# Kernel tuning notes

Measured on AMD Instinct MI355X. Metric: run time of the kernel, lower is better.

Reference implementation:

```python
import jax, jax.numpy as jnp
import numpy as np

KLD_BINS = 10
RATIO_KLD = 0.5
# categorical one-hot blocks in the 99-dim Adult encoding
BLOCKS = [(1, 8), (8, 24), (24, 31), (31, 45), (45, 51), (51, 53), (53, 55), (58, 99)]
CONT_COLS = np.array([0, 55, 56, 57])


def _cross_entropy(logits, onehot):
    # F.cross_entropy with targets = argmax of the one-hot block (mean over batch)
    logp = jax.nn.log_softmax(logits, axis=-1)
    return -jnp.mean(jnp.sum(onehot * logp, axis=-1))


def _kl_divergence(p, q):
    # np-style KL: sum p*log(p/q) over valid (nonzero) bins
    valid = (p > 0) & (q > 0)
    ratio = jnp.where(valid, p / jnp.where(valid, q, 1.0), 1.0)
    return jnp.sum(jnp.where(valid, p * jnp.log(ratio), 0.0))


def setup_inputs() -> dict:
    B = 262144
    key = jax.random.key(0)
    ks = jax.random.split(key, 16)
    data_decoded = jax.random.normal(ks[0], (B, 99), dtype=jnp.float32)
    # data_true: continuous columns + one-hot categorical blocks
    data_true = jnp.zeros((B, 99), dtype=jnp.float32)
    data_true = data_true.at[:, CONT_COLS].set(jax.random.normal(ks[1], (B, 4), dtype=jnp.float32))
    for j, (s, e) in enumerate(BLOCKS):
        lab = jax.random.randint(ks[2 + j], (B,), 0, e - s)
        data_true = data_true.at[:, s:e].set(jax.nn.one_hot(lab, e - s, dtype=jnp.float32))
    data_encoded = jax.random.normal(ks[11], (B, 12), dtype=jnp.float32)
    sex = jax.random.bernoulli(ks[12], 0.5, (B,)).astype(jnp.float32)
    data_encoded = data_encoded.at[:, 11].set(sex)  # column 11 of combined is the 0/1 sex neuron
    label_true = jax.random.normal(ks[13], (B, 2), dtype=jnp.float32)
    return {
        'data_encoded': data_encoded,
        'data_decoded': data_decoded,
        'data_true': data_true,
        'label_true': label_true,
        'batch_size': B,
    }


def reference(data_encoded, data_decoded, data_true, label_true, batch_size):
    # --- reconstruction MSE on continuous columns ---
    cc = jnp.asarray(CONT_COLS)
    mse_loss = jnp.sum(jnp.mean((data_decoded[:, cc] - data_true[:, cc]) ** 2, axis=0))
    # --- cross-entropy on each categorical block ---
    ce_loss = jnp.float32(0.0)
    for s, e in BLOCKS:
        ce_loss = ce_loss + _cross_entropy(data_decoded[:, s:e], data_true[:, s:e])
    # --- per-feature histogram KLD between male/female groups (no grad, as in torch via .numpy()) ---
    comb = jnp.concatenate([data_encoded, label_true], axis=1)  # [B, 14]
    feats = comb[:, :KLD_BINS]  # first 10 encoded features, [B, 10]
    mn = jnp.min(feats, axis=0)  # per-column min over full batch (torch .item())
    mx = jnp.max(feats, axis=0)
    width = jnp.maximum(mx - mn, 1e-12)
    # torch.histc bin index: floor((x-min)/(max-min)*bins), x==max -> last bin
    idx = jnp.clip(jnp.floor((feats - mn) / width * KLD_BINS).astype(jnp.int32), 0, KLD_BINS - 1)
    onehot = jax.nn.one_hot(idx, KLD_BINS, dtype=jnp.float32)  # [B, 10, bins]
    sexcol = comb[:, 11]
    m_mask = (sexcol == 0).astype(jnp.float32)
    f_mask = (sexcol == 1).astype(jnp.float32)
    m_count = jnp.maximum(jnp.sum(m_mask), 1.0)
    f_count = jnp.maximum(jnp.sum(f_mask), 1.0)
    m_hist = jnp.einsum('b,bik->ik', m_mask, onehot) / m_count  # [10, bins]
    f_hist = jnp.einsum('b,bik->ik', f_mask, onehot) / f_count
    kld = jax.lax.stop_gradient(_kl_divergence(m_hist, f_hist))
    alpha = RATIO_KLD
    multi_loss = (1.0 - alpha) * (mse_loss + ce_loss) + alpha * kld
    return (multi_loss, mse_loss, ce_loss, alpha * kld)
```

## Files before the change

### kernel.cpp

```cpp
#include <hip/hip_runtime.h>
#include <math.h>

#define B_ROWS 262144

#define WS_A 0
#define WS_B 2816
#define WS_C 28416
#define MAIN_BLOCKS 2048
#define N_TILES 4096

__device__ __forceinline__ unsigned int map_f(float x) {
  unsigned int b = __float_as_uint(x);
  return (b & 0x80000000u) ? ~b : (b | 0x80000000u);
}
__device__ __forceinline__ float unmap_f(unsigned int u) {
  unsigned int b = (u & 0x80000000u) ? (u ^ 0x80000000u) : ~u;
  return __uint_as_float(b);
}

__global__ __launch_bounds__(256) void k_minmax(const float* __restrict__ enc,
                                                unsigned int* __restrict__ ws) {
  int tid = threadIdx.x, bid = blockIdx.x;
  const float4* e4 = (const float4*)enc;
  float mn[10], mx[10];
  #pragma unroll
  for (int j = 0; j < 10; j++) { mn[j] = 1e30f; mx[j] = -1e30f; }
  unsigned int cm = 0, cf = 0;
  #pragma unroll
  for (int i = 0; i < 8; i++) {
    size_t g = (size_t)bid * 2048 + i * 256 + tid;
    float4 a = e4[g * 3 + 0], b = e4[g * 3 + 1], c = e4[g * 3 + 2];
    float v[12] = {a.x,a.y,a.z,a.w,b.x,b.y,b.z,b.w,c.x,c.y,c.z,c.w};
    #pragma unroll
    for (int j = 0; j < 10; j++) { mn[j] = fminf(mn[j], v[j]); mx[j] = fmaxf(mx[j], v[j]); }
    cm += (v[11] == 0.0f); cf += (v[11] == 1.0f);
  }
  #pragma unroll
  for (int off = 32; off; off >>= 1) {
    #pragma unroll
    for (int j = 0; j < 10; j++) {
      mn[j] = fminf(mn[j], __shfl_xor(mn[j], off));
      mx[j] = fmaxf(mx[j], __shfl_xor(mx[j], off));
    }
    cm += __shfl_xor(cm, off); cf += __shfl_xor(cf, off);
  }
  __shared__ float smn[4][10], smx[4][10];
  __shared__ unsigned int sc[4][2];
  int wave = tid >> 6, lane = tid & 63;
  if (lane == 0) {
    #pragma unroll
    for (int j = 0; j < 10; j++) { smn[wave][j] = mn[j]; smx[wave][j] = mx[j]; }
    sc[wave][0] = cm; sc[wave][1] = cf;
  }
  __syncthreads();
  unsigned int* out = ws + WS_A + bid * 22;
  if (tid < 10) {
    float m = fminf(fminf(smn[0][tid], smn[1][tid]), fminf(smn[2][tid], smn[3][tid]));
    out[tid] = map_f(m);
  } else if (tid < 20) {
    int j = tid - 10;
    float m = fmaxf(fmaxf(smx[0][j], smx[1][j]), fmaxf(smx[2][j], smx[3][j]));
    out[tid] = map_f(m);
  } else if (tid < 22) {
    int j = tid - 20;
    out[tid] = sc[0][j] + sc[1][j] + sc[2][j] + sc[3][j];
  }
}

__global__ __launch_bounds__(256) void k_hist(const float* __restrict__ enc,
                                              unsigned int* __restrict__ ws) {
  __shared__ float mnv[10], wid[10];
  __shared__ unsigned int h[200];
  int tid = threadIdx.x, bid = blockIdx.x;
  for (int i = tid; i < 200; i += 256) h[i] = 0u;
  if (tid < 10) {
    unsigned int umn = 0xFFFFFFFFu, umx = 0u;
    #pragma unroll 4
    for (int b = 0; b < 128; b++) {
      umn = min(umn, ws[WS_A + b * 22 + tid]);
      umx = max(umx, ws[WS_A + b * 22 + 10 + tid]);
    }
    float mn = unmap_f(umn);
    mnv[tid] = mn;
    wid[tid] = fmaxf(unmap_f(umx) - mn, 1e-12f);
  }
  __syncthreads();
  const float4* e4 = (const float4*)enc;
  #pragma unroll
  for (int i = 0; i < 8; i++) {
    size_t g = (size_t)bid * 2048 + i * 256 + tid;
    float4 a = e4[g * 3 + 0], b = e4[g * 3 + 1], c = e4[g * 3 + 2];
    float v[12] = {a.x,a.y,a.z,a.w,b.x,b.y,b.z,b.w,c.x,c.y,c.z,c.w};
    int base = (v[11] == 0.0f) ? 0 : ((v[11] == 1.0f) ? 100 : -1);
    if (base >= 0) {
      #pragma unroll
      for (int cc = 0; cc < 10; cc++) {
        float t = (v[cc] - mnv[cc]) / wid[cc] * 10.0f;
        int bi = min(max((int)floorf(t), 0), 9);
        atomicAdd(&h[base + cc * 10 + bi], 1u);
      }
    }
  }
  __syncthreads();
  if (tid < 200) ws[WS_B + bid * 200 + tid] = h[tid];
}

__global__ __launch_bounds__(64, 2) void k_main(const float* __restrict__ d,
                                                const float* __restrict__ t,
                                                unsigned int* __restrict__ ws) {
  __shared__ float lds[6336];
  int lane = threadIdx.x, bid = blockIdx.x;
  float mse = 0.f, dot = 0.f, ce = 0.f;

  for (int tileIdx = bid; tileIdx < N_TILES; tileIdx += MAIN_BLOCKS) {
    const float4* d4 = (const float4*)d + (size_t)tileIdx * 1584;
    const float4* t4 = (const float4*)t + (size_t)tileIdx * 1584;
    float4* l4 = (float4*)lds;
    #pragma unroll 5
    for (int f = lane; f < 1584; f += 64) {
      float4 xd = d4[f];
      float4 xt = t4[f];
      l4[f] = xd;
      int e = f * 4;
      int c = e - (e / 99) * 99;
      float dv[4] = {xd.x, xd.y, xd.z, xd.w};
      float tv[4] = {xt.x, xt.y, xt.z, xt.w};
      #pragma unroll
      for (int k = 0; k < 4; k++) {
        int cc = c + k;
        if (cc >= 99) cc -= 99;
        bool cont = (cc == 0) | ((unsigned)(cc - 55) <= 2u);
        float diff = dv[k] - tv[k];
        if (cont) mse += diff * diff;
        else      dot += tv[k] * dv[k];
      }
    }
    __syncthreads();
    const float* row = lds + lane * 99;
    float Z;
    Z = 0.f;
    #pragma unroll
    for (int c = 1; c < 8; c++) Z += __expf(row[c]);
    ce += __logf(Z);
    Z = 0.f;
    #pragma unroll
    for (int c = 8; c < 24; c++) Z += __expf(row[c]);
    ce += __logf(Z);
    Z = 0.f;
    #pragma unroll
    for (int c = 24; c < 31; c++) Z += __expf(row[c]);
    ce += __logf(Z);
    Z = 0.f;
    #pragma unroll
    for (int c = 31; c < 45; c++) Z += __expf(row[c]);
    ce += __logf(Z);
    Z = 0.f;
    #pragma unroll
    for (int c = 45; c < 51; c++) Z += __expf(row[c]);
    ce += __logf(Z);
    Z = 0.f;
    #pragma unroll
    for (int c = 51; c < 53; c++) Z += __expf(row[c]);
    ce += __logf(Z);
    Z = 0.f;
    #pragma unroll
    for (int c = 53; c < 55; c++) Z += __expf(row[c]);
    ce += __logf(Z);
    Z = 0.f;
    #pragma unroll
    for (int c = 58; c < 99; c++) Z += __expf(row[c]);
    ce += __logf(Z);
    __syncthreads();
  }

  #pragma unroll
  for (int off = 32; off; off >>= 1) {
    mse += __shfl_xor(mse, off);
    dot += __shfl_xor(dot, off);
    ce  += __shfl_xor(ce,  off);
  }
  if (lane == 0) {
    float* C = (float*)(ws + WS_C);
    C[bid]                   = mse;
    C[MAIN_BLOCKS + bid]     = dot;
    C[2 * MAIN_BLOCKS + bid] = ce;
  }
}

__global__ __launch_bounds__(256) void k_final(const unsigned int* __restrict__ ws,
                                               float* __restrict__ out) {
  __shared__ float h[200];
  __shared__ float part[256];
  __shared__ float red3[12];
  __shared__ float cnts[2];
  int tid = threadIdx.x;
  if (tid < 200) {
    unsigned int s = 0;
    #pragma unroll 4
    for (int b = 0; b < 128; b++) s += ws[WS_B + b * 200 + tid];
    h[tid] = (float)s;
  }
  if (tid == 200 || tid == 201) {
    unsigned int s = 0;
    #pragma unroll 4
    for (int b = 0; b < 128; b++) s += ws[WS_A + b * 22 + 20 + (tid - 200)];
    cnts[tid - 200] = fmaxf((float)s, 1.0f);
  }
  const float* C = (const float*)(ws + WS_C);
  float msum = 0.f, dsum = 0.f, csum = 0.f;
  for (int i = tid; i < MAIN_BLOCKS; i += 256) {
    msum += C[i]; dsum += C[MAIN_BLOCKS + i]; csum += C[2 * MAIN_BLOCKS + i];
  }
  #pragma unroll
  for (int off = 32; off; off >>= 1) {
    msum += __shfl_xor(msum, off);
    dsum += __shfl_xor(dsum, off);
    csum += __shfl_xor(csum, off);
  }
  int wave = tid >> 6, lane = tid & 63;
  if (lane == 0) { red3[wave] = msum; red3[4 + wave] = dsum; red3[8 + wave] = csum; }
  __syncthreads();
  float term = 0.f;
  if (tid < 100) {
    float mc = h[tid], fc = h[100 + tid];
    if (mc > 0.f && fc > 0.f) {
      float p = mc / cnts[0];
      float q = fc / cnts[1];
      term = p * logf(p / q);
    }
  }
  part[tid] = term;
  __syncthreads();
  for (int s = 128; s; s >>= 1) {
    if (tid < s) part[tid] += part[tid + s];
    __syncthreads();
  }
  if (tid == 0) {
    const float invB = 1.0f / (float)B_ROWS;
    float mse = (red3[0] + red3[1] + red3[2] + red3[3]) * invB;
    float dd  = (red3[4] + red3[5] + red3[6] + red3[7]);
    float cc  = (red3[8] + red3[9] + red3[10] + red3[11]);
    float ce  = (cc - dd) * invB;
    float akld = 0.5f * part[0];
    out[0] = 0.5f * (mse + ce) + akld;
    out[1] = mse;
    out[2] = ce;
    out[3] = akld;
  }
}

extern "C" void kernel_launch(void* const* d_in, const int* in_sizes, int n_in,
                              void* d_out, int out_size, void* d_ws, size_t ws_size,
                              hipStream_t stream) {
  const float* enc = (const float*)d_in[0];
  const float* dec = (const float*)d_in[1];
  const float* tru = (const float*)d_in[2];
  unsigned int* ws = (unsigned int*)d_ws;
  float* out = (float*)d_out;

  hipLaunchKernelGGL(k_minmax, dim3(128),         dim3(256), 0, stream, enc, ws);
  hipLaunchKernelGGL(k_hist,   dim3(128),         dim3(256), 0, stream, enc, ws);
  hipLaunchKernelGGL(k_main,   dim3(MAIN_BLOCKS), dim3(64),  0, stream, dec, tru, ws);
  hipLaunchKernelGGL(k_final,  dim3(1),           dim3(256), 0, stream, ws, out);
}
```

Baseline: 302.8 us.

## Load decoded tiles directly into LDS and batch target loads in registers

Decoded-data tiles are now copied into shared memory with the AMD global-to-LDS load builtin, which skips the register round trip. All 25 target float4 loads are issued up front into registers before a barrier, to increase memory-level parallelism. The grid shrinks from 2048 to 1536 blocks and the occupancy hint in launch bounds is dropped. The risks are higher register pressure from 100 floats of targets per lane, and an uneven tile distribution because 4096 tiles do not divide evenly over 1536 blocks.

```diff
diff --git a/kernel.cpp b/kernel.cpp
--- a/kernel.cpp
+++ b/kernel.cpp
@@ -6,7 +6,7 @@
 #define WS_A 0
 #define WS_B 2816
 #define WS_C 28416
-#define MAIN_BLOCKS 2048
+#define MAIN_BLOCKS 1536
 #define N_TILES 4096
 
 __device__ __forceinline__ unsigned int map_f(float x) {
@@ -105,9 +105,9 @@
   if (tid < 200) ws[WS_B + bid * 200 + tid] = h[tid];
 }
 
-__global__ __launch_bounds__(64, 2) void k_main(const float* __restrict__ d,
-                                                const float* __restrict__ t,
-                                                unsigned int* __restrict__ ws) {
+__global__ __launch_bounds__(64) void k_main(const float* __restrict__ d,
+                                             const float* __restrict__ t,
+                                             unsigned int* __restrict__ ws) {
   __shared__ float lds[6336];
   int lane = threadIdx.x, bid = blockIdx.x;
   float mse = 0.f, dot = 0.f, ce = 0.f;
@@ -115,27 +115,47 @@
   for (int tileIdx = bid; tileIdx < N_TILES; tileIdx += MAIN_BLOCKS) {
     const float4* d4 = (const float4*)d + (size_t)tileIdx * 1584;
     const float4* t4 = (const float4*)t + (size_t)tileIdx * 1584;
-    float4* l4 = (float4*)lds;
-    #pragma unroll 5
-    for (int f = lane; f < 1584; f += 64) {
-      float4 xd = d4[f];
-      float4 xt = t4[f];
-      l4[f] = xd;
-      int e = f * 4;
-      int c = e - (e / 99) * 99;
-      float dv[4] = {xd.x, xd.y, xd.z, xd.w};
-      float tv[4] = {xt.x, xt.y, xt.z, xt.w};
-      #pragma unroll
-      for (int k = 0; k < 4; k++) {
-        int cc = c + k;
-        if (cc >= 99) cc -= 99;
-        bool cont = (cc == 0) | ((unsigned)(cc - 55) <= 2u);
-        float diff = dv[k] - tv[k];
-        if (cont) mse += diff * diff;
-        else      dot += tv[k] * dv[k];
+
+    #pragma unroll
+    for (int it = 0; it < 25; ++it) {
+      int f = it * 64 + lane;
+      if (f < 1584)
+        __builtin_amdgcn_global_load_lds(
+            (const __attribute__((address_space(1))) void*)(d4 + f),
+            (__attribute__((address_space(3))) void*)(lds + it * 256),
+            16, 0, 0);
+    }
+    float4 tv[25];
+    #pragma unroll
+    for (int it = 0; it < 25; ++it) {
+      int f = it * 64 + lane;
+      if (f < 1584) tv[it] = t4[f];
+      else          tv[it] = make_float4(0.f, 0.f, 0.f, 0.f);
+    }
+    __syncthreads();
+
+    const float4* l4 = (const float4*)lds;
+    #pragma unroll
+    for (int it = 0; it < 25; ++it) {
+      int f = it * 64 + lane;
+      if (f < 1584) {
+        float4 xd = l4[f];
+        float4 xt = tv[it];
+        int e = f * 4;
+        int c = e - (e / 99) * 99;
+        float dv[4] = {xd.x, xd.y, xd.z, xd.w};
+        float tvv[4] = {xt.x, xt.y, xt.z, xt.w};
+        #pragma unroll
+        for (int k = 0; k < 4; k++) {
+          int cc = c + k;
+          if (cc >= 99) cc -= 99;
+          bool cont = (cc == 0) | ((unsigned)(cc - 55) <= 2u);
+          float diff = dv[k] - tvv[k];
+          if (cont) mse += diff * diff;
+          else      dot += tvv[k] * dv[k];
+        }
       }
     }
-    __syncthreads();
     const float* row = lds + lane * 99;
     float Z;
     Z = 0.f;
```

After: 273.8 us. 9.6% less time.

## Double-buffer main loss kernel with direct global-to-LDS async loads

Applied to the files above, without the earlier changes.

The main kernel now stages 32-row tiles of both the decoded and the true data straight into LDS using global_load_lds. It double-buffers them so the next tile's loads overlap compute on the current one, and synchronises with explicit vmcnt waits. The grid shrinks to 768 persistent single-wave blocks. Cross-entropy work is split between lane pairs, two lanes per row, so all 64 lanes stay busy. The aim is to hide memory latency and drop the register round trip and block barriers. In exchange the kernel depends on hand-counted vmcnt values and has no barrier between the LDS writes and reads, which is only safe within a single wave. The larger static LDS footprint may also cap occupancy.

```diff
diff --git a/kernel.cpp b/kernel.cpp
--- a/kernel.cpp
+++ b/kernel.cpp
@@ -6,8 +6,10 @@
 #define WS_A 0
 #define WS_B 2816
 #define WS_C 28416
-#define MAIN_BLOCKS 2048
-#define N_TILES 4096
+#define MAIN_BLOCKS 768
+#define TILE_ROWS 32
+#define N_TILES 8192
+#define TILE_F4 792
 
 __device__ __forceinline__ unsigned int map_f(float x) {
   unsigned int b = __float_as_uint(x);
@@ -105,22 +107,45 @@
   if (tid < 200) ws[WS_B + bid * 200 + tid] = h[tid];
 }
 
-__global__ __launch_bounds__(64, 2) void k_main(const float* __restrict__ d,
-                                                const float* __restrict__ t,
-                                                unsigned int* __restrict__ ws) {
-  __shared__ float lds[6336];
-  int lane = threadIdx.x, bid = blockIdx.x;
-  float mse = 0.f, dot = 0.f, ce = 0.f;
-
-  for (int tileIdx = bid; tileIdx < N_TILES; tileIdx += MAIN_BLOCKS) {
-    const float4* d4 = (const float4*)d + (size_t)tileIdx * 1584;
-    const float4* t4 = (const float4*)t + (size_t)tileIdx * 1584;
-    float4* l4 = (float4*)lds;
-    #pragma unroll 5
-    for (int f = lane; f < 1584; f += 64) {
-      float4 xd = d4[f];
-      float4 xt = t4[f];
-      l4[f] = xd;
+__shared__ float s_d0[3328], s_t0[3328], s_d1[3328], s_t1[3328];
+
+__device__ __forceinline__ void stage_tile(const float4* __restrict__ d4,
+                                           const float4* __restrict__ t4,
+                                           int tileIdx, float* ldsd, float* ldst,
+                                           int lane) {
+  const float4* ds = d4 + (size_t)tileIdx * TILE_F4;
+  const float4* ts = t4 + (size_t)tileIdx * TILE_F4;
+  #pragma unroll
+  for (int it = 0; it < 12; ++it)
+    __builtin_amdgcn_global_load_lds(
+        (const __attribute__((address_space(1))) void*)(ds + it * 64 + lane),
+        (__attribute__((address_space(3))) void*)(ldsd + it * 256), 16, 0, 0);
+  if (lane < 24)
+    __builtin_amdgcn_global_load_lds(
+        (const __attribute__((address_space(1))) void*)(ds + 768 + lane),
+        (__attribute__((address_space(3))) void*)(ldsd + 3072), 16, 0, 0);
+  #pragma unroll
+  for (int it = 0; it < 12; ++it)
+    __builtin_amdgcn_global_load_lds(
+        (const __attribute__((address_space(1))) void*)(ts + it * 64 + lane),
+        (__attribute__((address_space(3))) void*)(ldst + it * 256), 16, 0, 0);
+  if (lane < 24)
+    __builtin_amdgcn_global_load_lds(
+        (const __attribute__((address_space(1))) void*)(ts + 768 + lane),
+        (__attribute__((address_space(3))) void*)(ldst + 3072), 16, 0, 0);
+}
+
+__device__ __forceinline__ void compute_tile(const float* ldsd, const float* ldst,
+                                             int lane, float& mse, float& dot,
+                                             float& ce) {
+  const float4* ld4 = (const float4*)ldsd;
+  const float4* lt4 = (const float4*)ldst;
+  #pragma unroll
+  for (int it = 0; it < 13; ++it) {
+    int f = it * 64 + lane;
+    if (f < TILE_F4) {
+      float4 xd = ld4[f];
+      float4 xt = lt4[f];
       int e = f * 4;
       int c = e - (e / 99) * 99;
       float dv[4] = {xd.x, xd.y, xd.z, xd.w};
@@ -135,9 +160,11 @@
         else      dot += tv[k] * dv[k];
       }
     }
-    __syncthreads();
-    const float* row = lds + lane * 99;
-    float Z;
+  }
+  int r = lane >> 1;
+  const float* row = ldsd + r * 99;
+  float Z;
+  if ((lane & 1) == 0) {
     Z = 0.f;
     #pragma unroll
     for (int c = 1; c < 8; c++) Z += __expf(row[c]);
@@ -158,6 +185,7 @@
     #pragma unroll
     for (int c = 45; c < 51; c++) Z += __expf(row[c]);
     ce += __logf(Z);
+  } else {
     Z = 0.f;
     #pragma unroll
     for (int c = 51; c < 53; c++) Z += __expf(row[c]);
@@ -170,7 +198,31 @@
     #pragma unroll
     for (int c = 58; c < 99; c++) Z += __expf(row[c]);
     ce += __logf(Z);
-    __syncthreads();
+  }
+}
+
+__global__ __launch_bounds__(64) void k_main(const float* __restrict__ d,
+                                             const float* __restrict__ t,
+                                             unsigned int* __restrict__ ws) {
+  int lane = threadIdx.x, bid = blockIdx.x;
+  const float4* d4 = (const float4*)d;
+  const float4* t4 = (const float4*)t;
+  float mse = 0.f, dot = 0.f, ce = 0.f;
+
+  stage_tile(d4, t4, bid, s_d0, s_t0, lane);
+  int buf = 0;
+  for (int i = bid; i < N_TILES; i += MAIN_BLOCKS) {
+    int nxt = i + MAIN_BLOCKS;
+    if (nxt < N_TILES) {
+      stage_tile(d4, t4, nxt, buf ? s_d0 : s_d1, buf ? s_t0 : s_t1, lane);
+      asm volatile("s_waitcnt vmcnt(26)" ::: "memory");
+    } else {
+      asm volatile("s_waitcnt vmcnt(0)" ::: "memory");
+    }
+    if (buf) compute_tile(s_d1, s_t1, lane, mse, dot, ce);
+    else     compute_tile(s_d0, s_t0, lane, mse, dot, ce);
+    asm volatile("" ::: "memory");
+    buf ^= 1;
   }
 
   #pragma unroll
```

Result: slower. 358.8 us (+18.5%).

## Stream main-loss tiles per wave with direct global-to-LDS loads

Applied to the files above, without the earlier changes.

Rewrites k_main so each of four waves in a 256-thread block independently processes 16-row tiles. Both decoded and true data are loaded straight into LDS with global_load_lds and a vmcnt wait, replacing register loads followed by LDS stores and block-wide barriers. The aim is more loads in flight and no cross-wave synchronisation in this bandwidth-bound pass. In exchange, the per-row softmax work uses only 16 of 64 lanes per tile, and the partial-sum count written to the workspace and reduced in k_final grows to 3072 entries per term.

```diff
diff --git a/kernel.cpp b/kernel.cpp
--- a/kernel.cpp
+++ b/kernel.cpp
@@ -6,8 +6,11 @@
 #define WS_A 0
 #define WS_B 2816
 #define WS_C 28416
-#define MAIN_BLOCKS 2048
-#define N_TILES 4096
+#define MAIN_BLOCKS 768
+#define N_WAVES (MAIN_BLOCKS * 4)
+#define TILE_ROWS 16
+#define N_TILES 16384
+#define TILE_F4 396
 
 __device__ __forceinline__ unsigned int map_f(float x) {
   unsigned int b = __float_as_uint(x);
@@ -105,72 +108,103 @@
   if (tid < 200) ws[WS_B + bid * 200 + tid] = h[tid];
 }
 
-__global__ __launch_bounds__(64, 2) void k_main(const float* __restrict__ d,
-                                                const float* __restrict__ t,
-                                                unsigned int* __restrict__ ws) {
-  __shared__ float lds[6336];
-  int lane = threadIdx.x, bid = blockIdx.x;
+__global__ __launch_bounds__(256) void k_main(const float* __restrict__ d,
+                                              const float* __restrict__ t,
+                                              unsigned int* __restrict__ ws) {
+  __shared__ float sd[4 * 3168];
+  __shared__ float st[4 * 3168];
+  int tid = threadIdx.x, bid = blockIdx.x;
+  int wave = tid >> 6, lane = tid & 63;
+  float* ldsd = sd + wave * 3168;
+  float* ldst = st + wave * 3168;
+  const float4* ld4 = (const float4*)ldsd;
+  const float4* lt4 = (const float4*)ldst;
+  int gw = bid * 4 + wave;
+
   float mse = 0.f, dot = 0.f, ce = 0.f;
 
-  for (int tileIdx = bid; tileIdx < N_TILES; tileIdx += MAIN_BLOCKS) {
-    const float4* d4 = (const float4*)d + (size_t)tileIdx * 1584;
-    const float4* t4 = (const float4*)t + (size_t)tileIdx * 1584;
-    float4* l4 = (float4*)lds;
-    #pragma unroll 5
-    for (int f = lane; f < 1584; f += 64) {
-      float4 xd = d4[f];
-      float4 xt = t4[f];
-      l4[f] = xd;
-      int e = f * 4;
-      int c = e - (e / 99) * 99;
-      float dv[4] = {xd.x, xd.y, xd.z, xd.w};
-      float tv[4] = {xt.x, xt.y, xt.z, xt.w};
-      #pragma unroll
-      for (int k = 0; k < 4; k++) {
-        int cc = c + k;
-        if (cc >= 99) cc -= 99;
-        bool cont = (cc == 0) | ((unsigned)(cc - 55) <= 2u);
-        float diff = dv[k] - tv[k];
-        if (cont) mse += diff * diff;
-        else      dot += tv[k] * dv[k];
+  for (int tile = gw; tile < N_TILES; tile += N_WAVES) {
+    const float4* ds = (const float4*)d + (size_t)tile * TILE_F4;
+    const float4* ts = (const float4*)t + (size_t)tile * TILE_F4;
+    #pragma unroll
+    for (int it = 0; it < 6; ++it)
+      __builtin_amdgcn_global_load_lds(
+          (const __attribute__((address_space(1))) void*)(ds + it * 64 + lane),
+          (__attribute__((address_space(3))) void*)(ldsd + it * 1024 / 4), 16, 0, 0);
+    if (lane < 12)
+      __builtin_amdgcn_global_load_lds(
+          (const __attribute__((address_space(1))) void*)(ds + 384 + lane),
+          (__attribute__((address_space(3))) void*)(ldsd + 1536), 16, 0, 0);
+    #pragma unroll
+    for (int it = 0; it < 6; ++it)
+      __builtin_amdgcn_global_load_lds(
+          (const __attribute__((address_space(1))) void*)(ts + it * 64 + lane),
+          (__attribute__((address_space(3))) void*)(ldst + it * 1024 / 4), 16, 0, 0);
+    if (lane < 12)
+      __builtin_amdgcn_global_load_lds(
+          (const __attribute__((address_space(1))) void*)(ts + 384 + lane),
+          (__attribute__((address_space(3))) void*)(ldst + 1536), 16, 0, 0);
+
+    asm volatile("s_waitcnt vmcnt(0)" ::: "memory");
+
+    #pragma unroll
+    for (int it = 0; it < 7; ++it) {
+      int f = it * 64 + lane;
+      if (f < TILE_F4) {
+        float4 xd = ld4[f];
+        float4 xt = lt4[f];
+        int e = f * 4;
+        int c = e - (e / 99) * 99;
+        float dv[4] = {xd.x, xd.y, xd.z, xd.w};
+        float tv[4] = {xt.x, xt.y, xt.z, xt.w};
+        #pragma unroll
+        for (int k = 0; k < 4; k++) {
+          int cc = c + k;
+          if (cc >= 99) cc -= 99;
+          bool cont = (cc == 0) | ((unsigned)(cc - 55) <= 2u);
+          float diff = dv[k] - tv[k];
+          if (cont) mse += diff * diff;
+          else      dot += tv[k] * dv[k];
+        }
       }
     }
-    __syncthreads();
-    const float* row = lds + lane * 99;
-    float Z;
-    Z = 0.f;
-    #pragma unroll
-    for (int c = 1; c < 8; c++) Z += __expf(row[c]);
-    ce += __logf(Z);
-    Z = 0.f;
-    #pragma unroll
-    for (int c = 8; c < 24; c++) Z += __expf(row[c]);
-    ce += __logf(Z);
-    Z = 0.f;
-    #pragma unroll
-    for (int c = 24; c < 31; c++) Z += __expf(row[c]);
-    ce += __logf(Z);
-    Z = 0.f;
-    #pragma unroll
-    for (int c = 31; c < 45; c++) Z += __expf(row[c]);
-    ce += __logf(Z);
-    Z = 0.f;
-    #pragma unroll
-    for (int c = 45; c < 51; c++) Z += __expf(row[c]);
-    ce += __logf(Z);
-    Z = 0.f;
-    #pragma unroll
-    for (int c = 51; c < 53; c++) Z += __expf(row[c]);
-    ce += __logf(Z);
-    Z = 0.f;
-    #pragma unroll
-    for (int c = 53; c < 55; c++) Z += __expf(row[c]);
-    ce += __logf(Z);
-    Z = 0.f;
-    #pragma unroll
-    for (int c = 58; c < 99; c++) Z += __expf(row[c]);
-    ce += __logf(Z);
-    __syncthreads();
+    if (lane < TILE_ROWS) {
+      const float* row = ldsd + lane * 99;
+      float Z;
+      Z = 0.f;
+      #pragma unroll
+      for (int c = 1; c < 8; c++) Z += __expf(row[c]);
+      ce += __logf(Z);
+      Z = 0.f;
+      #pragma unroll
+      for (int c = 8; c < 24; c++) Z += __expf(row[c]);
+      ce += __logf(Z);
+      Z = 0.f;
+      #pragma unroll
+      for (int c = 24; c < 31; c++) Z += __expf(row[c]);
+      ce += __logf(Z);
+      Z = 0.f;
+      #pragma unroll
+      for (int c = 31; c < 45; c++) Z += __expf(row[c]);
+      ce += __logf(Z);
+      Z = 0.f;
+      #pragma unroll
+      for (int c = 45; c < 51; c++) Z += __expf(row[c]);
+      ce += __logf(Z);
+      Z = 0.f;
+      #pragma unroll
+      for (int c = 51; c < 53; c++) Z += __expf(row[c]);
+      ce += __logf(Z);
+      Z = 0.f;
+      #pragma unroll
+      for (int c = 53; c < 55; c++) Z += __expf(row[c]);
+      ce += __logf(Z);
+      Z = 0.f;
+      #pragma unroll
+      for (int c = 58; c < 99; c++) Z += __expf(row[c]);
+      ce += __logf(Z);
+    }
+    asm volatile("s_waitcnt lgkmcnt(0)" ::: "memory");
   }
 
   #pragma unroll
@@ -181,9 +215,9 @@
   }
   if (lane == 0) {
     float* C = (float*)(ws + WS_C);
-    C[bid]                   = mse;
-    C[MAIN_BLOCKS + bid]     = dot;
-    C[2 * MAIN_BLOCKS + bid] = ce;
+    C[gw]               = mse;
+    C[N_WAVES + gw]     = dot;
+    C[2 * N_WAVES + gw] = ce;
   }
 }
 
@@ -208,8 +242,8 @@
   }
   const float* C = (const float*)(ws + WS_C);
   float msum = 0.f, dsum = 0.f, csum = 0.f;
-  for (int i = tid; i < MAIN_BLOCKS; i += 256) {
-    msum += C[i]; dsum += C[MAIN_BLOCKS + i]; csum += C[2 * MAIN_BLOCKS + i];
+  for (int i = tid; i < N_WAVES; i += 256) {
+    msum += C[i]; dsum += C[N_WAVES + i]; csum += C[2 * N_WAVES + i];
   }
   #pragma unroll
   for (int off = 32; off; off >>= 1) {
@@ -260,6 +294,6 @@
 
   hipLaunchKernelGGL(k_minmax, dim3(128),         dim3(256), 0, stream, enc, ws);
   hipLaunchKernelGGL(k_hist,   dim3(128),         dim3(256), 0, stream, enc, ws);
-  hipLaunchKernelGGL(k_main,   dim3(MAIN_BLOCKS), dim3(64),  0, stream, dec, tru, ws);
+  hipLaunchKernelGGL(k_main,   dim3(MAIN_BLOCKS), dim3(256), 0, stream, dec, tru, ws);
   hipLaunchKernelGGL(k_final,  dim3(1),           dim3(256), 0, stream, ws, out);
 }
```

New measurement: 271.3 us. 1.12x faster.
